# Optimization experiments

Measured on AMD Instinct MI355X. Metric: run time of the kernel, lower is better.

## Reference

```python
import jax, jax.numpy as jnp
import numpy as np

N = 1572864          # total anchors (P2-P7 pyramid on 1024x1024, 18 anchors/loc)
K = 4096             # fixed NMS candidate budget (jit-compatible top-k prefilter)
IMG_H, IMG_W = 1024, 1024
IOU_THR = 0.1
SCORE_THR = 0.5
BBOX_STD = np.array([0.1, 0.1, 0.2, 0.2], dtype=np.float32)  # RetinaNet BBoxTransform std


def setup_inputs() -> dict:
    key = jax.random.key(0)
    k1, k2, k3, k4 = jax.random.split(key, 4)
    classification = jax.random.uniform(k1, (1, N, 2), dtype=jnp.float32)
    regression = jax.random.normal(k2, (1, N, 4), dtype=jnp.float32)
    ctr = jax.random.uniform(k3, (1, N, 2), dtype=jnp.float32, minval=0.0, maxval=1024.0)
    wh = jax.random.uniform(k4, (1, N, 2), dtype=jnp.float32, minval=16.0, maxval=256.0)
    anchors = jnp.concatenate([ctr - 0.5 * wh, ctr + 0.5 * wh], axis=-1)  # [1,N,4] x1y1x2y2
    return {"classification": classification, "regression": regression,
            "anchors": anchors, "H": IMG_H, "W": IMG_W}


def _decode_clip(anchors, deltas):
    # BBoxTransform: anchors/deltas [1,N,4] -> boxes [N,4], then ClipBoxes to image.
    a = anchors[0]
    d = deltas[0] * jnp.asarray(BBOX_STD)
    w = a[:, 2] - a[:, 0]
    h = a[:, 3] - a[:, 1]
    cx = a[:, 0] + 0.5 * w
    cy = a[:, 1] + 0.5 * h
    pcx = cx + d[:, 0] * w
    pcy = cy + d[:, 1] * h
    pw = jnp.exp(d[:, 2]) * w
    ph = jnp.exp(d[:, 3]) * h
    boxes = jnp.stack([pcx - 0.5 * pw, pcy - 0.5 * ph,
                       pcx + 0.5 * pw, pcy + 0.5 * ph], axis=-1)
    lo = jnp.zeros((4,), jnp.float32)
    hi = jnp.asarray([IMG_W, IMG_H, IMG_W, IMG_H], jnp.float32)
    return jnp.clip(boxes, lo, hi)


def _iou_matrix(b):
    # b: [K,4] -> [K,K] pairwise IoU
    area = (b[:, 2] - b[:, 0]) * (b[:, 3] - b[:, 1])
    lt = jnp.maximum(b[:, None, :2], b[None, :, :2])
    rb = jnp.minimum(b[:, None, 2:], b[None, :, 2:])
    wh = jnp.clip(rb - lt, 0.0)
    inter = wh[..., 0] * wh[..., 1]
    return inter / (area[:, None] + area[None, :] - inter + 1e-8)


def reference(classification, regression, anchors, H, W):
    boxes = _decode_clip(anchors, regression)          # [N,4]
    scores = classification[0, :, 1]                   # [N]
    masked = jnp.where(scores > SCORE_THR, scores, 0.0)
    top_s, order = jax.lax.top_k(masked, K)            # score-sorted candidates
    cand = boxes[order]                                # [K,4]
    iou = _iou_matrix(cand)                            # [K,K]
    valid = top_s > 0.0
    idx = jnp.arange(K)

    def body(keep, i):
        suppress = (iou[i] > IOU_THR) & keep[i] & (idx > i)
        return keep & ~suppress, None

    keep, _ = jax.lax.scan(body, valid, idx)
    keepf = keep.astype(cand.dtype)
    # rescale boxes from model img_shape back to input H,W (factor 1 when H=W=1024)
    scale = jnp.asarray([W / IMG_W, H / IMG_H, W / IMG_W, H / IMG_H], jnp.float32)
    out_boxes = cand * scale * keepf[:, None]
    out_scores = top_s * keepf
    return jnp.concatenate([out_boxes, out_scores[:, None]], axis=-1)  # [K,5]
```

## Files before the change

kernel.cpp:

```cpp
#include <hip/hip_runtime.h>
#include <cstdint>

#define N_TOT 1572864
#define KSEL 4096
#define CAP 8192
#define BINS 4096
#define SCORE_THR 0.5f
#define IOU_THR 0.1f
#define STREAM_BLOCKS 512
#define STAGE 512

__device__ inline uint64_t readlane64(uint64_t v, int lane) {
    uint32_t lo = (uint32_t)__builtin_amdgcn_readlane((int)(uint32_t)v, lane);
    uint32_t hi = (uint32_t)__builtin_amdgcn_readlane((int)(uint32_t)(v >> 32), lane);
    return ((uint64_t)hi << 32) | lo;
}

__global__ void k_init(uint32_t* hist, uint32_t* ctrs, float* topScore) {
    int i = blockIdx.x * blockDim.x + threadIdx.x;
    if (i < BINS) hist[i] = 0;
    if (i < 16) ctrs[i] = 0;
    if (i < KSEL) topScore[i] = 0.0f;
}

__global__ void k_hist(const float4* __restrict__ cls4, uint32_t* __restrict__ hist) {
    int i = blockIdx.x * blockDim.x + threadIdx.x;
    int stride = gridDim.x * blockDim.x;
    for (; i < N_TOT / 2; i += stride) {
        float4 c = cls4[i];
        if (c.y > SCORE_THR) {
            uint32_t bin = (__float_as_uint(c.y) - 0x3F000000u) >> 11;
            if (bin >= BINS) bin = BINS - 1;
            atomicAdd(&hist[bin], 1u);
        }
        if (c.w > SCORE_THR) {
            uint32_t bin = (__float_as_uint(c.w) - 0x3F000000u) >> 11;
            if (bin >= BINS) bin = BINS - 1;
            atomicAdd(&hist[bin], 1u);
        }
    }
}

__global__ __launch_bounds__(1024) void k_thresh(const uint32_t* __restrict__ hist,
                                                 uint32_t* __restrict__ ctrs) {
    __shared__ uint32_t s_suf[1024];
    int t = threadIdx.x;
    uint32_t l0 = hist[t*4+0], l1 = hist[t*4+1], l2 = hist[t*4+2], l3 = hist[t*4+3];
    s_suf[t] = l0 + l1 + l2 + l3;
    __syncthreads();
    for (int off = 1; off < 1024; off <<= 1) {
        uint32_t v = (t + off < 1024) ? s_suf[t + off] : 0u;
        __syncthreads();
        s_suf[t] += v;
        __syncthreads();
    }
    uint32_t snext = (t < 1023) ? s_suf[t + 1] : 0u;
    uint32_t suf3 = snext + l3;
    uint32_t suf2 = suf3 + l2;
    uint32_t suf1 = suf2 + l1;
    uint32_t suf0 = suf1 + l0;
    uint32_t sufs[5] = {suf0, suf1, suf2, suf3, snext};
    #pragma unroll
    for (int q = 0; q < 4; q++) {
        if (sufs[q] >= KSEL && sufs[q+1] < KSEL) ctrs[1] = (uint32_t)(t*4 + q);
    }
    if (t == 0 && s_suf[0] < KSEL) ctrs[1] = 0;
}

__global__ void k_gather(const float4* __restrict__ cls4, uint32_t* __restrict__ ctrs,
                         uint64_t* __restrict__ keys) {
    __shared__ uint32_t s_cnt;
    __shared__ uint32_t s_base;
    __shared__ uint64_t s_stage[STAGE];
    if (threadIdx.x == 0) s_cnt = 0;
    __syncthreads();

    uint32_t T = ctrs[1];
    uint32_t basebits = 0x3F000000u + (T << 11);
    int i = blockIdx.x * blockDim.x + threadIdx.x;
    int stride = gridDim.x * blockDim.x;
    for (; i < N_TOT / 2; i += stride) {
        float4 c = cls4[i];
        #pragma unroll
        for (int h = 0; h < 2; h++) {
            float s = h ? c.w : c.y;
            uint32_t idx = 2u * (uint32_t)i + (uint32_t)h;
            if (s > SCORE_THR) {
                uint32_t b = __float_as_uint(s);
                if (b >= basebits) {
                    uint64_t key = ((uint64_t)b << 32) | (uint32_t)(~idx);
                    uint32_t p = atomicAdd(&s_cnt, 1u);
                    if (p < STAGE) s_stage[p] = key;
                    else {
                        uint32_t g = atomicAdd(&ctrs[0], 1u);
                        if (g < CAP) keys[g] = key;
                    }
                }
            }
        }
    }
    __syncthreads();
    uint32_t n = s_cnt < STAGE ? s_cnt : STAGE;
    if (threadIdx.x == 0 && n > 0) s_base = atomicAdd(&ctrs[0], n);
    __syncthreads();
    for (uint32_t q = threadIdx.x; q < n; q += blockDim.x) {
        uint32_t g = s_base + q;
        if (g < CAP) keys[g] = s_stage[q];
    }
}

__global__ void k_rankdec(const uint64_t* __restrict__ keys, const uint32_t* __restrict__ ctrs,
                          const float* __restrict__ anchors, const float* __restrict__ reg,
                          float* __restrict__ topScore, float* __restrict__ boxes,
                          float* __restrict__ areas) {
    __shared__ uint64_t s_keys[256];
    uint32_t M = ctrs[0]; if (M > CAP) M = CAP;
    int j = blockIdx.x * blockDim.x + threadIdx.x;
    uint64_t myKey = (j < (int)M) ? keys[j] : 0ull;
    uint32_t rank = 0;
    for (uint32_t base = 0; base < M; base += 256) {
        uint32_t idx = base + threadIdx.x;
        s_keys[threadIdx.x] = (idx < M) ? keys[idx] : 0ull;
        __syncthreads();
        uint32_t lim = min(256u, M - base);
        for (uint32_t q = 0; q < lim; q++)
            rank += (s_keys[q] > myKey) ? 1u : 0u;
        __syncthreads();
    }
    if (j < (int)M && rank < KSEL) {
        uint32_t srcIdx = ~((uint32_t)(myKey & 0xFFFFFFFFull));
        topScore[rank] = __uint_as_float((uint32_t)(myKey >> 32));
        float4 a = *reinterpret_cast<const float4*>(&anchors[(size_t)srcIdx * 4]);
        float4 dd = *reinterpret_cast<const float4*>(&reg[(size_t)srcIdx * 4]);
        float d0 = __fmul_rn(dd.x, 0.1f);
        float d1 = __fmul_rn(dd.y, 0.1f);
        float d2 = __fmul_rn(dd.z, 0.2f);
        float d3 = __fmul_rn(dd.w, 0.2f);
        float w  = __fsub_rn(a.z, a.x);
        float h  = __fsub_rn(a.w, a.y);
        float cx = __fadd_rn(a.x, __fmul_rn(0.5f, w));
        float cy = __fadd_rn(a.y, __fmul_rn(0.5f, h));
        float pcx = __fadd_rn(cx, __fmul_rn(d0, w));
        float pcy = __fadd_rn(cy, __fmul_rn(d1, h));
        float pw = __fmul_rn((float)exp((double)d2), w);
        float ph = __fmul_rn((float)exp((double)d3), h);
        float x0 = __fsub_rn(pcx, __fmul_rn(0.5f, pw));
        float y0 = __fsub_rn(pcy, __fmul_rn(0.5f, ph));
        float x1 = __fadd_rn(pcx, __fmul_rn(0.5f, pw));
        float y1 = __fadd_rn(pcy, __fmul_rn(0.5f, ph));
        x0 = fminf(fmaxf(x0, 0.0f), 1024.0f);
        y0 = fminf(fmaxf(y0, 0.0f), 1024.0f);
        x1 = fminf(fmaxf(x1, 0.0f), 1024.0f);
        y1 = fminf(fmaxf(y1, 0.0f), 1024.0f);
        *reinterpret_cast<float4*>(&boxes[(size_t)rank * 4]) = make_float4(x0, y0, x1, y1);
        areas[rank] = __fmul_rn(__fsub_rn(x1, x0), __fsub_rn(y1, y0));
    }
}

__global__ void k_mask(const float* __restrict__ boxes, const float* __restrict__ areas,
                       unsigned long long* __restrict__ rowmask) {
    int bi = blockIdx.y, bj = blockIdx.x;
    int t = threadIdx.x;
    if (bj < bi) {
        rowmask[(size_t)(bi * 64 + t) * 64 + bj] = 0ull;
        return;
    }
    __shared__ float s_box[64][4];
    __shared__ float s_area[64];
    int r0 = bi * 64 + t;
    s_box[t][0] = boxes[r0 * 4 + 0];
    s_box[t][1] = boxes[r0 * 4 + 1];
    s_box[t][2] = boxes[r0 * 4 + 2];
    s_box[t][3] = boxes[r0 * 4 + 3];
    s_area[t] = areas[r0];
    __syncthreads();
    int j = bj * 64 + t;
    float jx0 = boxes[j * 4 + 0], jy0 = boxes[j * 4 + 1], jx1 = boxes[j * 4 + 2], jy1 = boxes[j * 4 + 3];
    float ja = areas[j];
    unsigned long long myword = 0ull;
    #pragma unroll 4
    for (int r = 0; r < 64; r++) {
        int i = bi * 64 + r;
        float w = __fsub_rn(fminf(s_box[r][2], jx1), fmaxf(s_box[r][0], jx0));
        float h = __fsub_rn(fminf(s_box[r][3], jy1), fmaxf(s_box[r][1], jy0));
        w = fmaxf(w, 0.0f); h = fmaxf(h, 0.0f);
        float inter = __fmul_rn(w, h);
        float denom = __fadd_rn(__fsub_rn(__fadd_rn(s_area[r], ja), inter), 1e-8f);
        float iou = __fdiv_rn(inter, denom);
        bool sup = (iou > IOU_THR) && (j > i);
        unsigned long long b = __ballot(sup);
        if (t == r) myword = b;
    }
    rowmask[(size_t)(bi * 64 + t) * 64 + bj] = myword;
}

__device__ __forceinline__ void issue_rows(const unsigned long long* __restrict__ rowmask,
                                           int b, int half, int w, uint64_t (&buf)[32]) {
    const unsigned long long* p = rowmask + (size_t)(b * 64 + half * 32) * 64 + w;
    #pragma unroll
    for (int i = 0; i < 32; i++) buf[i] = p[(size_t)i * 64];
}

__device__ __forceinline__ uint64_t or_rows(uint64_t kwhalf, const uint64_t (&buf)[32]) {
    uint64_t acc = 0ull;
    #pragma unroll
    for (int i = 0; i < 32; i++) {
        uint64_t m = (uint64_t)0 - ((kwhalf >> i) & 1ull);
        acc |= buf[i] & m;
    }
    return acc;
}

__global__ __launch_bounds__(64, 1) void k_reduce(const float* __restrict__ topScore,
                         const unsigned long long* __restrict__ rowmask,
                         const float* __restrict__ boxes,
                         const int* __restrict__ Hp, const int* __restrict__ Wp,
                         float* __restrict__ out) {
    int w = threadIdx.x;
    uint64_t keep = 0ull;
    #pragma unroll
    for (int c = 0; c < 64; c += 4) {
        float4 s4 = *reinterpret_cast<const float4*>(&topScore[w * 64 + c]);
        keep |= ((uint64_t)(s4.x > 0.0f) << (c + 0))
             |  ((uint64_t)(s4.y > 0.0f) << (c + 1))
             |  ((uint64_t)(s4.z > 0.0f) << (c + 2))
             |  ((uint64_t)(s4.w > 0.0f) << (c + 3));
    }

    uint64_t A[32], B[32];
    issue_rows(rowmask, 0, 0, w, A);
    uint64_t dg0 = rowmask[(size_t)(0 * 64 + w) * 64 + 0];
    uint64_t dg1 = rowmask[(size_t)(1 * 64 + w) * 64 + 1];

    for (int b = 0; b < 64; b++) {
        issue_rows(rowmask, b, 1, w, B);
        uint64_t diag = dg0;
        dg0 = dg1;
        int nb = (b + 2 < 64) ? (b + 2) : 63;
        dg1 = rowmask[(size_t)(nb * 64 + w) * 64 + nb];

        uint32_t klo = (uint32_t)__builtin_amdgcn_readlane((int)(uint32_t)keep, b);
        uint32_t khi = (uint32_t)__builtin_amdgcn_readlane((int)(uint32_t)(keep >> 32), b);
        uint64_t kw = ((uint64_t)khi << 32) | klo;
        uint64_t rem = kw;
        while (rem) {
            int i = __builtin_ctzll(rem);
            rem &= rem - 1;
            uint64_t row = readlane64(diag, i);
            kw &= ~row;
            rem &= ~row;
        }

        uint64_t acc = or_rows(kw, A);
        if (b + 1 < 64) issue_rows(rowmask, b + 1, 0, w, A);
        acc |= or_rows(kw >> 32, B);
        keep &= ~acc;
    }

    float sx = (float)((double)Wp[0] / 1024.0);
    float sy = (float)((double)Hp[0] / 1024.0);
    for (int c = 0; c < 64; c++) {
        int k = w * 64 + c;
        float f = ((keep >> c) & 1ull) ? 1.0f : 0.0f;
        float4 bx = *reinterpret_cast<const float4*>(&boxes[(size_t)k * 4]);
        out[k * 5 + 0] = __fmul_rn(__fmul_rn(bx.x, sx), f);
        out[k * 5 + 1] = __fmul_rn(__fmul_rn(bx.y, sy), f);
        out[k * 5 + 2] = __fmul_rn(__fmul_rn(bx.z, sx), f);
        out[k * 5 + 3] = __fmul_rn(__fmul_rn(bx.w, sy), f);
        out[k * 5 + 4] = __fmul_rn(topScore[k], f);
    }
}

extern "C" void kernel_launch(void* const* d_in, const int* in_sizes, int n_in,
                              void* d_out, int out_size, void* d_ws, size_t ws_size,
                              hipStream_t stream) {
    (void)in_sizes; (void)n_in; (void)out_size; (void)ws_size;
    const float4* cls4   = (const float4*)d_in[0];
    const float* reg     = (const float*)d_in[1];
    const float* anchors = (const float*)d_in[2];
    const int* Hp        = (const int*)d_in[3];
    const int* Wp        = (const int*)d_in[4];
    float* out = (float*)d_out;

    char* ws = (char*)d_ws;
    size_t off = 0;
    auto alloc = [&](size_t bytes) {
        char* p = ws + off;
        off = (off + bytes + 255) & ~(size_t)255;
        return p;
    };
    uint32_t* hist   = (uint32_t*)alloc(BINS * 4);
    uint32_t* ctrs   = (uint32_t*)alloc(64);
    uint64_t* keys   = (uint64_t*)alloc((size_t)CAP * 8);
    float* topScore  = (float*)alloc(KSEL * 4);
    float* boxes     = (float*)alloc(KSEL * 4 * 4);
    float* areas     = (float*)alloc(KSEL * 4);
    unsigned long long* rowmask = (unsigned long long*)alloc((size_t)KSEL * 64 * 8);

    k_init<<<16, 256, 0, stream>>>(hist, ctrs, topScore);
    k_hist<<<STREAM_BLOCKS, 256, 0, stream>>>(cls4, hist);
    k_thresh<<<1, 1024, 0, stream>>>(hist, ctrs);
    k_gather<<<STREAM_BLOCKS, 256, 0, stream>>>(cls4, ctrs, keys);
    k_rankdec<<<CAP / 256, 256, 0, stream>>>(keys, ctrs, anchors, reg, topScore, boxes, areas);
    dim3 mg(64, 64);
    k_mask<<<mg, 64, 0, stream>>>(boxes, areas, rowmask);
    k_reduce<<<1, 64, 0, stream>>>(topScore, rowmask, boxes, Hp, Wp, out);
}
```

Baseline: 263.8 us.

## Stage NMS row-mask blocks into LDS with a dedicated producer wave

The serial NMS reduce kernel now runs two waves: one issues async global-to-LDS loads (global_load_lds) of the next 32KB row-mask block into a double buffer, while the other runs the greedy suppression for the current block reading from LDS. This replaces register-prefetched global loads, aiming to hide memory latency in the single-block serial stage. It adds a block barrier per iteration. It also relies on those async LDS loads being complete at the barrier, without an explicit wait on the load counter.

```diff
diff --git a/kernel.cpp b/kernel.cpp
--- a/kernel.cpp
+++ b/kernel.cpp
@@ -14,6 +14,13 @@
     uint32_t lo = (uint32_t)__builtin_amdgcn_readlane((int)(uint32_t)v, lane);
     uint32_t hi = (uint32_t)__builtin_amdgcn_readlane((int)(uint32_t)(v >> 32), lane);
     return ((uint64_t)hi << 32) | lo;
+}
+
+__device__ __forceinline__ void gload16(const void* gsrc, void* lds_uniform) {
+    __builtin_amdgcn_global_load_lds(
+        (const __attribute__((address_space(1))) void*)gsrc,
+        (__attribute__((address_space(3))) void*)lds_uniform,
+        16, 0, 0);
 }
 
 __global__ void k_init(uint32_t* hist, uint32_t* ctrs, float* topScore) {
@@ -194,80 +201,87 @@
     rowmask[(size_t)(bi * 64 + t) * 64 + bj] = myword;
 }
 
-__device__ __forceinline__ void issue_rows(const unsigned long long* __restrict__ rowmask,
-                                           int b, int half, int w, uint64_t (&buf)[32]) {
-    const unsigned long long* p = rowmask + (size_t)(b * 64 + half * 32) * 64 + w;
-    #pragma unroll
-    for (int i = 0; i < 32; i++) buf[i] = p[(size_t)i * 64];
-}
-
-__device__ __forceinline__ uint64_t or_rows(uint64_t kwhalf, const uint64_t (&buf)[32]) {
-    uint64_t acc = 0ull;
-    #pragma unroll
-    for (int i = 0; i < 32; i++) {
-        uint64_t m = (uint64_t)0 - ((kwhalf >> i) & 1ull);
-        acc |= buf[i] & m;
-    }
-    return acc;
-}
-
-__global__ __launch_bounds__(64, 1) void k_reduce(const float* __restrict__ topScore,
+__global__ __launch_bounds__(128, 1) void k_reduce(const float* __restrict__ topScore,
                          const unsigned long long* __restrict__ rowmask,
                          const float* __restrict__ boxes,
                          const int* __restrict__ Hp, const int* __restrict__ Wp,
                          float* __restrict__ out) {
-    int w = threadIdx.x;
+    __shared__ uint64_t lds[2][4096];
+    int tid = threadIdx.x;
+    int wid = tid >> 6;
+    int l = tid & 63;
+
+    const char* rmbytes = (const char*)rowmask;
+
+    if (wid == 1) {
+        #pragma unroll
+        for (int k = 0; k < 32; k++) {
+            gload16(rmbytes + (size_t)0 * 32768 + k * 1024 + l * 16,
+                    (char*)&lds[0][0] + k * 1024);
+        }
+    }
+
     uint64_t keep = 0ull;
-    #pragma unroll
-    for (int c = 0; c < 64; c += 4) {
-        float4 s4 = *reinterpret_cast<const float4*>(&topScore[w * 64 + c]);
-        keep |= ((uint64_t)(s4.x > 0.0f) << (c + 0))
-             |  ((uint64_t)(s4.y > 0.0f) << (c + 1))
-             |  ((uint64_t)(s4.z > 0.0f) << (c + 2))
-             |  ((uint64_t)(s4.w > 0.0f) << (c + 3));
-    }
-
-    uint64_t A[32], B[32];
-    issue_rows(rowmask, 0, 0, w, A);
-    uint64_t dg0 = rowmask[(size_t)(0 * 64 + w) * 64 + 0];
-    uint64_t dg1 = rowmask[(size_t)(1 * 64 + w) * 64 + 1];
+    if (wid == 0) {
+        #pragma unroll
+        for (int c = 0; c < 64; c += 4) {
+            float4 s4 = *reinterpret_cast<const float4*>(&topScore[l * 64 + c]);
+            keep |= ((uint64_t)(s4.x > 0.0f) << (c + 0))
+                 |  ((uint64_t)(s4.y > 0.0f) << (c + 1))
+                 |  ((uint64_t)(s4.z > 0.0f) << (c + 2))
+                 |  ((uint64_t)(s4.w > 0.0f) << (c + 3));
+        }
+    }
+    __syncthreads();
 
     for (int b = 0; b < 64; b++) {
-        issue_rows(rowmask, b, 1, w, B);
-        uint64_t diag = dg0;
-        dg0 = dg1;
-        int nb = (b + 2 < 64) ? (b + 2) : 63;
-        dg1 = rowmask[(size_t)(nb * 64 + w) * 64 + nb];
-
-        uint32_t klo = (uint32_t)__builtin_amdgcn_readlane((int)(uint32_t)keep, b);
-        uint32_t khi = (uint32_t)__builtin_amdgcn_readlane((int)(uint32_t)(keep >> 32), b);
-        uint64_t kw = ((uint64_t)khi << 32) | klo;
-        uint64_t rem = kw;
-        while (rem) {
-            int i = __builtin_ctzll(rem);
-            rem &= rem - 1;
-            uint64_t row = readlane64(diag, i);
-            kw &= ~row;
-            rem &= ~row;
-        }
-
-        uint64_t acc = or_rows(kw, A);
-        if (b + 1 < 64) issue_rows(rowmask, b + 1, 0, w, A);
-        acc |= or_rows(kw >> 32, B);
-        keep &= ~acc;
-    }
-
-    float sx = (float)((double)Wp[0] / 1024.0);
-    float sy = (float)((double)Hp[0] / 1024.0);
-    for (int c = 0; c < 64; c++) {
-        int k = w * 64 + c;
-        float f = ((keep >> c) & 1ull) ? 1.0f : 0.0f;
-        float4 bx = *reinterpret_cast<const float4*>(&boxes[(size_t)k * 4]);
-        out[k * 5 + 0] = __fmul_rn(__fmul_rn(bx.x, sx), f);
-        out[k * 5 + 1] = __fmul_rn(__fmul_rn(bx.y, sy), f);
-        out[k * 5 + 2] = __fmul_rn(__fmul_rn(bx.z, sx), f);
-        out[k * 5 + 3] = __fmul_rn(__fmul_rn(bx.w, sy), f);
-        out[k * 5 + 4] = __fmul_rn(topScore[k], f);
+        if (wid == 1) {
+            if (b + 1 < 64) {
+                int s = (b + 1) & 1;
+                #pragma unroll
+                for (int k = 0; k < 32; k++) {
+                    gload16(rmbytes + (size_t)(b + 1) * 32768 + k * 1024 + l * 16,
+                            (char*)&lds[s][0] + k * 1024);
+                }
+            }
+        } else {
+            const uint64_t* slot = &lds[b & 1][0];
+            uint64_t diag = slot[l * 64 + b];
+            uint32_t klo = (uint32_t)__builtin_amdgcn_readlane((int)(uint32_t)keep, b);
+            uint32_t khi = (uint32_t)__builtin_amdgcn_readlane((int)(uint32_t)(keep >> 32), b);
+            uint64_t kw = ((uint64_t)khi << 32) | klo;
+            uint64_t rem = kw;
+            while (rem) {
+                int i = __builtin_ctzll(rem);
+                rem &= rem - 1;
+                uint64_t row = readlane64(diag, i);
+                kw &= ~row;
+                rem &= ~row;
+            }
+            uint64_t acc = 0ull;
+            #pragma unroll 8
+            for (int r = 0; r < 64; r++) {
+                uint64_t m = (uint64_t)0 - ((kw >> r) & 1ull);
+                acc |= slot[r * 64 + l] & m;
+            }
+            keep &= ~acc;
+        }
+        __syncthreads();
+    }
+
+    if (wid == 0) {
+        float sx = (float)((double)Wp[0] / 1024.0);
+        float sy = (float)((double)Hp[0] / 1024.0);
+        for (int c = 0; c < 64; c++) {
+            int k = l * 64 + c;
+            float f = ((keep >> c) & 1ull) ? 1.0f : 0.0f;
+            float4 bx = *reinterpret_cast<const float4*>(&boxes[(size_t)k * 4]);
+            out[k * 5 + 0] = __fmul_rn(__fmul_rn(bx.x, sx), f);
+            out[k * 5 + 1] = __fmul_rn(__fmul_rn(bx.y, sy), f);
+            out[k * 5 + 2] = __fmul_rn(__fmul_rn(bx.z, sx), f);
+            out[k * 5 + 3] = __fmul_rn(__fmul_rn(bx.w, sy), f);
+            out[k * 5 + 4] = __fmul_rn(topScore[k], f);
+        }
     }
 }
 
@@ -304,5 +318,5 @@
     k_rankdec<<<CAP / 256, 256, 0, stream>>>(keys, ctrs, anchors, reg, topScore, boxes, areas);
     dim3 mg(64, 64);
     k_mask<<<mg, 64, 0, stream>>>(boxes, areas, rowmask);
-    k_reduce<<<1, 64, 0, stream>>>(topScore, rowmask, boxes, Hp, Wp, out);
-}
+    k_reduce<<<1, 128, 0, stream>>>(topScore, rowmask, boxes, Hp, Wp, out);
+}
```

Result: slower. 273.6 us (+3.7%).

## Spread NMS mask reduction across 16 wavefronts with LDS partial ORs

Applied to the files above, without the earlier changes.

The serial NMS reduction kernel is widened from one wavefront to sixteen. Each wave loads four rows of each 64-row block through inline-asm global loads kept four blocks in flight, and ORs its partial suppression masks through shared memory. Diagonal blocks and keep words are staged in LDS. Grid sizes for the histogram and gather kernels also change. The aim is to cut the latency-bound single-wave loop, at the cost of two barriers per block step and fragile hand-written asm waitcnt ordering.

```diff
diff --git a/kernel.cpp b/kernel.cpp
--- a/kernel.cpp
+++ b/kernel.cpp
@@ -7,7 +7,6 @@
 #define BINS 4096
 #define SCORE_THR 0.5f
 #define IOU_THR 0.1f
-#define STREAM_BLOCKS 512
 #define STAGE 512
 
 __device__ inline uint64_t readlane64(uint64_t v, int lane) {
@@ -194,74 +193,104 @@
     rowmask[(size_t)(bi * 64 + t) * 64 + bj] = myword;
 }
 
-__device__ __forceinline__ void issue_rows(const unsigned long long* __restrict__ rowmask,
-                                           int b, int half, int w, uint64_t (&buf)[32]) {
-    const unsigned long long* p = rowmask + (size_t)(b * 64 + half * 32) * 64 + w;
-    #pragma unroll
-    for (int i = 0; i < 32; i++) buf[i] = p[(size_t)i * 64];
-}
-
-__device__ __forceinline__ uint64_t or_rows(uint64_t kwhalf, const uint64_t (&buf)[32]) {
-    uint64_t acc = 0ull;
-    #pragma unroll
-    for (int i = 0; i < 32; i++) {
-        uint64_t m = (uint64_t)0 - ((kwhalf >> i) & 1ull);
-        acc |= buf[i] & m;
-    }
-    return acc;
-}
-
-__global__ __launch_bounds__(64, 1) void k_reduce(const float* __restrict__ topScore,
+#define ISSUEB(p, nb) { \
+    uint64_t blk = rm_base + (uint64_t)(nb) * 32768ull; \
+    asm volatile("global_load_dwordx2 %0, %1, %2" : "=v"(p##0) : "v"(voff0), "s"(blk)); \
+    asm volatile("global_load_dwordx2 %0, %1, %2" : "=v"(p##1) : "v"(voff1), "s"(blk)); \
+    asm volatile("global_load_dwordx2 %0, %1, %2" : "=v"(p##2) : "v"(voff2), "s"(blk)); \
+    asm volatile("global_load_dwordx2 %0, %1, %2" : "=v"(p##3) : "v"(voff3), "s"(blk)); \
+}
+
+#define STEP(bidx, p) { \
+    int b_ = (bidx); \
+    uint64_t kb = s_keep[b_]; \
+    uint64_t diag = s_diag[b_][w]; \
+    uint64_t kw = kb, rem = kb; \
+    while (rem) { \
+        int i_ = __builtin_ctzll(rem); \
+        rem &= rem - 1ull; \
+        uint64_t row = readlane64(diag, i_); \
+        kw &= ~row; rem &= ~row; \
+    } \
+    uint64_t kwv; \
+    asm volatile("s_waitcnt vmcnt(12)" \
+        : "=v"(kwv), "+v"(p##0), "+v"(p##1), "+v"(p##2), "+v"(p##3) : "0"(kw)); \
+    uint64_t part = (p##0 & (0ull - ((kwv >> (g * 4 + 0)) & 1ull))) \
+                  | (p##1 & (0ull - ((kwv >> (g * 4 + 1)) & 1ull))) \
+                  | (p##2 & (0ull - ((kwv >> (g * 4 + 2)) & 1ull))) \
+                  | (p##3 & (0ull - ((kwv >> (g * 4 + 3)) & 1ull))); \
+    s_part[g][w] = part; \
+    int nb_ = b_ + 4; if (nb_ > 63) nb_ = 63; \
+    ISSUEB(p, nb_) \
+    asm volatile("s_waitcnt lgkmcnt(0)" ::: "memory"); \
+    __builtin_amdgcn_s_barrier(); \
+    __builtin_amdgcn_sched_barrier(0); \
+    uint64_t acc = 0ull; \
+    _Pragma("unroll") \
+    for (int gg = 0; gg < 16; gg++) acc |= s_part[gg][w]; \
+    uint64_t nk = s_keep[w] & ~acc; \
+    s_keep[w] = nk; \
+    asm volatile("s_waitcnt lgkmcnt(0)" ::: "memory"); \
+    __builtin_amdgcn_s_barrier(); \
+    __builtin_amdgcn_sched_barrier(0); \
+}
+
+__global__ __launch_bounds__(1024, 1) void k_reduce(const float* __restrict__ topScore,
                          const unsigned long long* __restrict__ rowmask,
                          const float* __restrict__ boxes,
                          const int* __restrict__ Hp, const int* __restrict__ Wp,
                          float* __restrict__ out) {
-    int w = threadIdx.x;
-    uint64_t keep = 0ull;
+    __shared__ uint64_t s_diag[64][64];
+    __shared__ uint64_t s_part[16][64];
+    __shared__ uint64_t s_keep[64];
+    int t = threadIdx.x;
+    int w = t & 63;
+    int g = t >> 6;
+
+    uint32_t voff0 = (uint32_t)((g * 256 + 0 * 64 + w) * 8);
+    uint32_t voff1 = (uint32_t)((g * 256 + 1 * 64 + w) * 8);
+    uint32_t voff2 = (uint32_t)((g * 256 + 2 * 64 + w) * 8);
+    uint32_t voff3 = (uint32_t)((g * 256 + 3 * 64 + w) * 8);
+    uint64_t rm_base = (uint64_t)(uintptr_t)rowmask;
+
     #pragma unroll
-    for (int c = 0; c < 64; c += 4) {
-        float4 s4 = *reinterpret_cast<const float4*>(&topScore[w * 64 + c]);
-        keep |= ((uint64_t)(s4.x > 0.0f) << (c + 0))
-             |  ((uint64_t)(s4.y > 0.0f) << (c + 1))
-             |  ((uint64_t)(s4.z > 0.0f) << (c + 2))
-             |  ((uint64_t)(s4.w > 0.0f) << (c + 3));
-    }
-
-    uint64_t A[32], B[32];
-    issue_rows(rowmask, 0, 0, w, A);
-    uint64_t dg0 = rowmask[(size_t)(0 * 64 + w) * 64 + 0];
-    uint64_t dg1 = rowmask[(size_t)(1 * 64 + w) * 64 + 1];
-
-    for (int b = 0; b < 64; b++) {
-        issue_rows(rowmask, b, 1, w, B);
-        uint64_t diag = dg0;
-        dg0 = dg1;
-        int nb = (b + 2 < 64) ? (b + 2) : 63;
-        dg1 = rowmask[(size_t)(nb * 64 + w) * 64 + nb];
-
-        uint32_t klo = (uint32_t)__builtin_amdgcn_readlane((int)(uint32_t)keep, b);
-        uint32_t khi = (uint32_t)__builtin_amdgcn_readlane((int)(uint32_t)(keep >> 32), b);
-        uint64_t kw = ((uint64_t)khi << 32) | klo;
-        uint64_t rem = kw;
-        while (rem) {
-            int i = __builtin_ctzll(rem);
-            rem &= rem - 1;
-            uint64_t row = readlane64(diag, i);
-            kw &= ~row;
-            rem &= ~row;
+    for (int q = 0; q < 4; q++) {
+        int bb = g * 4 + q;
+        s_diag[bb][w] = rowmask[(size_t)(bb * 64 + w) * 64 + bb];
+    }
+    if (g == 0) {
+        uint64_t keep = 0ull;
+        #pragma unroll
+        for (int c = 0; c < 64; c += 4) {
+            float4 s4 = *reinterpret_cast<const float4*>(&topScore[w * 64 + c]);
+            keep |= ((uint64_t)(s4.x > 0.0f) << (c + 0))
+                 |  ((uint64_t)(s4.y > 0.0f) << (c + 1))
+                 |  ((uint64_t)(s4.z > 0.0f) << (c + 2))
+                 |  ((uint64_t)(s4.w > 0.0f) << (c + 3));
         }
-
-        uint64_t acc = or_rows(kw, A);
-        if (b + 1 < 64) issue_rows(rowmask, b + 1, 0, w, A);
-        acc |= or_rows(kw >> 32, B);
-        keep &= ~acc;
-    }
+        s_keep[w] = keep;
+    }
+    __syncthreads();
+
+    uint64_t a0, a1, a2, a3, b0, b1, b2, b3;
+    uint64_t c0, c1, c2, c3, d0, d1, d2, d3;
+    ISSUEB(a, 0) ISSUEB(b, 1) ISSUEB(c, 2) ISSUEB(d, 3)
+    __builtin_amdgcn_sched_barrier(0);
+
+    for (int bb = 0; bb < 64; bb += 4) {
+        STEP(bb + 0, a)
+        STEP(bb + 1, b)
+        STEP(bb + 2, c)
+        STEP(bb + 3, d)
+    }
+    asm volatile("s_waitcnt vmcnt(0)" ::: "memory");
 
     float sx = (float)((double)Wp[0] / 1024.0);
     float sy = (float)((double)Hp[0] / 1024.0);
-    for (int c = 0; c < 64; c++) {
-        int k = w * 64 + c;
-        float f = ((keep >> c) & 1ull) ? 1.0f : 0.0f;
+    #pragma unroll
+    for (int q = 0; q < 4; q++) {
+        int k = t * 4 + q;
+        float f = ((s_keep[k >> 6] >> (k & 63)) & 1ull) ? 1.0f : 0.0f;
         float4 bx = *reinterpret_cast<const float4*>(&boxes[(size_t)k * 4]);
         out[k * 5 + 0] = __fmul_rn(__fmul_rn(bx.x, sx), f);
         out[k * 5 + 1] = __fmul_rn(__fmul_rn(bx.y, sy), f);
@@ -298,11 +327,11 @@
     unsigned long long* rowmask = (unsigned long long*)alloc((size_t)KSEL * 64 * 8);
 
     k_init<<<16, 256, 0, stream>>>(hist, ctrs, topScore);
-    k_hist<<<STREAM_BLOCKS, 256, 0, stream>>>(cls4, hist);
+    k_hist<<<2048, 256, 0, stream>>>(cls4, hist);
     k_thresh<<<1, 1024, 0, stream>>>(hist, ctrs);
-    k_gather<<<STREAM_BLOCKS, 256, 0, stream>>>(cls4, ctrs, keys);
+    k_gather<<<256, 256, 0, stream>>>(cls4, ctrs, keys);
     k_rankdec<<<CAP / 256, 256, 0, stream>>>(keys, ctrs, anchors, reg, topScore, boxes, areas);
     dim3 mg(64, 64);
     k_mask<<<mg, 64, 0, stream>>>(boxes, areas, rowmask);
-    k_reduce<<<1, 64, 0, stream>>>(topScore, rowmask, boxes, Hp, Wp, out);
-}
+    k_reduce<<<1, 1024, 0, stream>>>(topScore, rowmask, boxes, Hp, Wp, out);
+}
```

After: 252.4 us. -4.3%, faster.
